# Performance work log

Measured on AMD Instinct MI355X. Metric: run time of the kernel, lower is better.

## Reference

```python
import jax, jax.numpy as jnp
import numpy as np

H = 16  # num_heads
D = 64  # head_dim


def setup_inputs() -> dict:
    key = jax.random.key(0)
    ks = jax.random.split(key, 9)
    B, S, E = 2, 2048, 1024
    scale = 1.0 / np.sqrt(E)
    return {
        "hidden_states": jax.random.normal(ks[0], (B, S, E), jnp.float32),
        "bias": jax.random.normal(ks[1], (1, H, S, S), jnp.float32) * 0.02,
        "Wq": jax.random.normal(ks[2], (E, E), jnp.float32) * scale,
        "bq": jax.random.normal(ks[3], (E,), jnp.float32) * 0.02,
        "Wk": jax.random.normal(ks[4], (E, E), jnp.float32) * scale,
        "bk": jax.random.normal(ks[5], (E,), jnp.float32) * 0.02,
        "Wv": jax.random.normal(ks[6], (E, E), jnp.float32) * scale,
        "bv": jax.random.normal(ks[7], (E,), jnp.float32) * 0.02,
        "Wo": jax.random.normal(ks[8], (E, E), jnp.float32) * scale,
    }


def _split_heads(x, B, S):
    # (B, S, E) -> (B, H, S, D)
    return x.reshape(B, S, H, D).transpose(0, 2, 1, 3)


def reference(hidden_states, bias, Wq, bq, Wk, bk, Wv, bv, Wo):
    B, S, E = hidden_states.shape
    # nn.Linear: y = x @ W^T + b
    q = _split_heads(hidden_states @ Wq.T + bq, B, S)
    k = _split_heads(hidden_states @ Wk.T + bk, B, S)
    v = _split_heads(hidden_states @ Wv.T + bv, B, S)
    scores = jnp.einsum("bhqd,bhkd->bhqk", q, k) / jnp.sqrt(jnp.asarray(D, q.dtype))
    scores = scores + bias  # bias [1,H,S,S] broadcasts over batch (matches .repeat)
    attn = jax.nn.softmax(scores, axis=-1)
    out = jnp.einsum("bhqk,bhkd->bhqd", attn, v)
    out = out.transpose(0, 2, 1, 3).reshape(B, S, E)
    return out @ Wo.T
```

## Files before the change

kernel.cpp:

```cpp
#include <hip/hip_runtime.h>
#include <hip/hip_bf16.h>


typedef __attribute__((ext_vector_type(8))) __bf16 bf16x8;
typedef __attribute__((ext_vector_type(4))) float f32x4;

__device__ __forceinline__ void gl2lds16(const void* g, void* l) {
    __builtin_amdgcn_global_load_lds(
        (const __attribute__((address_space(1))) void*)g,
        (__attribute__((address_space(3))) void*)l, 16, 0, 0);
}

__global__ __launch_bounds__(256) void prep(
    const float* __restrict__ hs, const float* __restrict__ Wq,
    const float* __restrict__ Wk, const float* __restrict__ Wv,
    const float* __restrict__ Wo,
    __bf16* __restrict__ hsb, __bf16* __restrict__ wqb, __bf16* __restrict__ wkb,
    __bf16* __restrict__ wvb, __bf16* __restrict__ wohb, __bf16* __restrict__ wolb)
{
    size_t i = (size_t)blockIdx.x * 256 + threadIdx.x;
    const float* s; __bf16 *d1, *d2 = nullptr; size_t off;
    if (i < 1048576)      { s = hs; d1 = hsb; off = i; }
    else if (i < 1310720) { s = Wq; d1 = wqb; off = i - 1048576; }
    else if (i < 1572864) { s = Wk; d1 = wkb; off = i - 1310720; }
    else if (i < 1835008) { s = Wv; d1 = wvb; off = i - 1572864; }
    else                  { s = Wo; d1 = wohb; d2 = wolb; off = i - 1835008; }
    float4 v = *(const float4*)(s + off * 4);
    union { __bf16 b[4]; uint2 u; } ph;
    ph.b[0] = (__bf16)v.x; ph.b[1] = (__bf16)v.y;
    ph.b[2] = (__bf16)v.z; ph.b[3] = (__bf16)v.w;
    *(uint2*)(d1 + off * 4) = ph.u;
    if (d2) {
        union { __bf16 b[4]; uint2 u; } pl;
        pl.b[0] = (__bf16)(v.x - (float)ph.b[0]);
        pl.b[1] = (__bf16)(v.y - (float)ph.b[1]);
        pl.b[2] = (__bf16)(v.z - (float)ph.b[2]);
        pl.b[3] = (__bf16)(v.w - (float)ph.b[3]);
        *(uint2*)(d2 + off * 4) = pl.u;
    }
}

__global__ __launch_bounds__(256, 3) void gemm_qkv(
    const __bf16* __restrict__ hsb, const __bf16* __restrict__ wqb,
    const __bf16* __restrict__ wkb, const __bf16* __restrict__ wvb,
    const float* __restrict__ bq, const float* __restrict__ bk, const float* __restrict__ bv,
    __bf16* __restrict__ qo, __bf16* __restrict__ ko, __bf16* __restrict__ vTo)
{
    __shared__ alignas(16) __bf16 As[128][32];
    __shared__ alignas(16) __bf16 Ws[128][32];
    const int tid = threadIdx.x;
    const int w = tid >> 6, lane = tid & 63, quad = lane >> 4, l = lane & 15;
    const int blk = blockIdx.x;
    const int proj = blk >> 8;
    const int loc = blk & 255;
    int bm, bn;
    const __bf16 *Ap, *Wp; const float* bp;
    if (proj == 0)      { Ap = hsb; Wp = wqb; bp = bq; bm = (loc >> 3) << 7; bn = (loc & 7) << 7; }
    else if (proj == 1) { Ap = hsb; Wp = wkb; bp = bk; bm = (loc >> 3) << 7; bn = (loc & 7) << 7; }
    else                { Ap = wvb; Wp = hsb; bp = bv; bm = (loc & 7) << 7; bn = (loc >> 3) << 7; }
    const int wm = (w >> 1) << 6, wn = (w & 1) << 6;
    const int seg_r = lane >> 2, seg_c = (lane & 3) << 3;

    f32x4 acc[4][4];
#pragma unroll
    for (int i = 0; i < 4; ++i)
#pragma unroll
        for (int j = 0; j < 4; ++j) acc[i][j] = f32x4{0.f, 0.f, 0.f, 0.f};

    for (int k0 = 0; k0 < 1024; k0 += 32) {
        __syncthreads();
#pragma unroll
        for (int j = 0; j < 2; ++j) {
            int seg = w * 2 + j;
            int row = seg * 16 + seg_r;
            gl2lds16(Ap + (size_t)(bm + row) * 1024 + k0 + seg_c,
                     (char*)As + seg * 1024 + lane * 16);
            gl2lds16(Wp + (size_t)(bn + row) * 1024 + k0 + seg_c,
                     (char*)Ws + seg * 1024 + lane * 16);
        }
        __syncthreads();
        bf16x8 af[4], bfr[4];
#pragma unroll
        for (int t = 0; t < 4; ++t) {
            af[t]  = *(const bf16x8*)&As[wm + t * 16 + l][quad * 8];
            bfr[t] = *(const bf16x8*)&Ws[wn + t * 16 + l][quad * 8];
        }
#pragma unroll
        for (int mt = 0; mt < 4; ++mt)
#pragma unroll
            for (int nt = 0; nt < 4; ++nt)
                acc[mt][nt] = __builtin_amdgcn_mfma_f32_16x16x32_bf16(
                    af[mt], bfr[nt], acc[mt][nt], 0, 0, 0);
    }

    if (proj < 2) {
        __bf16* dst = proj ? ko : qo;
        const float scale = proj ? 1.0f : 0.125f;
        float bcol[4];
#pragma unroll
        for (int nt = 0; nt < 4; ++nt) bcol[nt] = bp[bn + wn + nt * 16 + l];
#pragma unroll
        for (int mt = 0; mt < 4; ++mt)
#pragma unroll
            for (int r = 0; r < 4; ++r) {
                int m = bm + wm + mt * 16 + quad * 4 + r;
                int b_ = m >> 11, s = m & 2047;
#pragma unroll
                for (int nt = 0; nt < 4; ++nt) {
                    int n = bn + wn + nt * 16 + l;
                    int h = n >> 6, d = n & 63;
                    dst[(((size_t)(b_ * 16 + h) * 2048 + s) << 6) + d] =
                        (__bf16)((acc[mt][nt][r] + bcol[nt]) * scale);
                }
            }
    } else {
#pragma unroll
        for (int mt = 0; mt < 4; ++mt)
#pragma unroll
            for (int r = 0; r < 4; ++r) {
                int im = bm + wm + mt * 16 + quad * 4 + r;
                int h = im >> 6, d = im & 63;
                float bm_ = bp[im];
#pragma unroll
                for (int nt = 0; nt < 4; ++nt) {
                    int in = bn + wn + nt * 16 + l;
                    int b_ = in >> 11, s = in & 2047;
                    vTo[(((size_t)(b_ * 16 + h) * 64 + d) << 11) + s] =
                        (__bf16)(acc[mt][nt][r] + bm_);
                }
            }
    }
}

__global__ __launch_bounds__(256, 2) void flash_attn_mfma(
    const __bf16* __restrict__ q, const __bf16* __restrict__ k,
    const __bf16* __restrict__ vT, const float* __restrict__ bias,
    __bf16* __restrict__ attn_hi, __bf16* __restrict__ attn_lo)
{
    constexpr int S = 2048;
    __shared__ alignas(16) unsigned char smem[33792];
    __bf16 (*Ks)[64]  = (__bf16(*)[64])(smem);
    __bf16 (*VTs)[64] = (__bf16(*)[64])(smem + 8192);
    __bf16 (*Ps)[68]  = (__bf16(*)[68])(smem + 16384);
    __bf16 (*Qs)[64]  = (__bf16(*)[64])(smem + 16384);

    const int tid = threadIdx.x;
    const int b = blockIdx.x, h = blockIdx.y, qt = blockIdx.z;
    const int bh = b * 16 + h;
    const int q0 = qt * 128;
    const int w = tid >> 6, lane = tid & 63, quad = lane >> 4, l = lane & 15;

    const __bf16* Qp = q + ((size_t)bh * S + q0) * 64;
#pragma unroll
    for (int j = 0; j < 4; ++j) {
        int P = (w * 4 + j) * 64 + lane;
        int row = P >> 3, pblk = P & 7;
        int lblk = pblk ^ (row & 7);
        gl2lds16(Qp + row * 64 + lblk * 8, (char*)Qs + (size_t)P * 16);
    }
    __syncthreads();

    bf16x8 qf[2][2];
#pragma unroll
    for (int rt = 0; rt < 2; ++rt)
#pragma unroll
        for (int ks = 0; ks < 2; ++ks) {
            int row = w * 32 + rt * 16 + l;
            qf[rt][ks] = *(const bf16x8*)&Qs[row][((ks * 4 + quad) ^ (row & 7)) * 8];
        }

    float l_[2][4];
    f32x4 o_[2][4];
#pragma unroll
    for (int rt = 0; rt < 2; ++rt)
#pragma unroll
        for (int r = 0; r < 4; ++r) {
            l_[rt][r] = 0.0f;
            o_[rt][r] = f32x4{0.f, 0.f, 0.f, 0.f};
        }

    const __bf16* Kp0 = k + (size_t)bh * S * 64;
    const __bf16* Vp0 = vT + (size_t)bh * 64 * S;
    const float* Bp0 = bias + (size_t)h * S * S + (size_t)q0 * S;

    for (int kt = 0; kt < S / 64; ++kt) {
        f32x4 sc[2][4];
#pragma unroll
        for (int rt = 0; rt < 2; ++rt)
#pragma unroll
            for (int r = 0; r < 4; ++r) {
                const float* bp = Bp0 + (size_t)(w * 32 + rt * 16 + quad * 4 + r) * S
                                + kt * 64 + l;
#pragma unroll
                for (int ct = 0; ct < 4; ++ct) sc[rt][ct][r] = bp[ct * 16];
            }

        __syncthreads();
        const __bf16* Kt = Kp0 + kt * 64 * 64;
        const __bf16* Vt = Vp0 + kt * 64;
#pragma unroll
        for (int j = 0; j < 2; ++j) {
            int P = (w * 2 + j) * 64 + lane;
            int row = P >> 3, pblk = P & 7;
            int lblk = pblk ^ (row & 7);
            gl2lds16(Kt + row * 64 + lblk * 8,        (char*)Ks  + (size_t)P * 16);
            gl2lds16(Vt + (size_t)row * S + lblk * 8, (char*)VTs + (size_t)P * 16);
        }
        __syncthreads();

#pragma unroll
        for (int ct = 0; ct < 4; ++ct) {
            int krow = ct * 16 + l;
            bf16x8 b0 = *(const bf16x8*)&Ks[krow][((0 + quad) ^ (l & 7)) * 8];
            bf16x8 b1 = *(const bf16x8*)&Ks[krow][((4 + quad) ^ (l & 7)) * 8];
            sc[0][ct] = __builtin_amdgcn_mfma_f32_16x16x32_bf16(qf[0][0], b0, sc[0][ct], 0, 0, 0);
            sc[0][ct] = __builtin_amdgcn_mfma_f32_16x16x32_bf16(qf[0][1], b1, sc[0][ct], 0, 0, 0);
            sc[1][ct] = __builtin_amdgcn_mfma_f32_16x16x32_bf16(qf[1][0], b0, sc[1][ct], 0, 0, 0);
            sc[1][ct] = __builtin_amdgcn_mfma_f32_16x16x32_bf16(qf[1][1], b1, sc[1][ct], 0, 0, 0);
        }

#pragma unroll
        for (int rt = 0; rt < 2; ++rt)
#pragma unroll
            for (int r = 0; r < 4; ++r) {
                int row = w * 32 + rt * 16 + quad * 4 + r;
                float ps = 0.f;
#pragma unroll
                for (int ct = 0; ct < 4; ++ct) {
                    float p = __expf(sc[rt][ct][r] - 8.0f);
                    Ps[row][ct * 16 + l] = (__bf16)p;
                    ps += p;
                }
                l_[rt][r] += ps;
            }

#pragma unroll
        for (int ks = 0; ks < 2; ++ks) {
            bf16x8 pa0 = *(const bf16x8*)&Ps[w * 32 + l][ks * 32 + quad * 8];
            bf16x8 pa1 = *(const bf16x8*)&Ps[w * 32 + 16 + l][ks * 32 + quad * 8];
#pragma unroll
            for (int dt = 0; dt < 4; ++dt) {
                bf16x8 vb = *(const bf16x8*)&VTs[dt * 16 + l][((ks * 4 + quad) ^ (l & 7)) * 8];
                o_[0][dt] = __builtin_amdgcn_mfma_f32_16x16x32_bf16(pa0, vb, o_[0][dt], 0, 0, 0);
                o_[1][dt] = __builtin_amdgcn_mfma_f32_16x16x32_bf16(pa1, vb, o_[1][dt], 0, 0, 0);
            }
        }
    }

#pragma unroll
    for (int rt = 0; rt < 2; ++rt)
#pragma unroll
        for (int r = 0; r < 4; ++r) {
            float ps = l_[rt][r];
            ps += __shfl_xor(ps, 1);
            ps += __shfl_xor(ps, 2);
            ps += __shfl_xor(ps, 4);
            ps += __shfl_xor(ps, 8);
            float linv = 1.0f / ps;
            int row = q0 + w * 32 + rt * 16 + quad * 4 + r;
            size_t base = (size_t)(b * S + row) * 1024 + h * 64;
#pragma unroll
            for (int dt = 0; dt < 4; ++dt) {
                float x = o_[rt][dt][r] * linv;
                __bf16 hi = (__bf16)x;
                attn_hi[base + dt * 16 + l] = hi;
                attn_lo[base + dt * 16 + l] = (__bf16)(x - (float)hi);
            }
        }
}

__global__ __launch_bounds__(256, 3) void gemm_out(
    const __bf16* __restrict__ ah, const __bf16* __restrict__ al,
    const __bf16* __restrict__ wh, const __bf16* __restrict__ wl,
    float* __restrict__ C)
{
    __shared__ alignas(16) __bf16 Ah[64][32], Al[64][32];
    __shared__ alignas(16) __bf16 Wh[128][32], Wl[128][32];
    const int tid = threadIdx.x;
    const int w = tid >> 6, lane = tid & 63, quad = lane >> 4, l = lane & 15;
    const int bm = (int)(blockIdx.x >> 3) << 6;
    const int bn = (int)(blockIdx.x & 7) << 7;
    const int wm = (w >> 1) << 5, wn = (w & 1) << 6;
    const int seg_r = lane >> 2, seg_c = (lane & 3) << 3;

    f32x4 acc[2][4];
#pragma unroll
    for (int i = 0; i < 2; ++i)
#pragma unroll
        for (int j = 0; j < 4; ++j) acc[i][j] = f32x4{0.f, 0.f, 0.f, 0.f};

    for (int k0 = 0; k0 < 1024; k0 += 32) {
        __syncthreads();
        {
            int row = w * 16 + seg_r;
            gl2lds16(ah + (size_t)(bm + row) * 1024 + k0 + seg_c,
                     (char*)Ah + w * 1024 + lane * 16);
            gl2lds16(al + (size_t)(bm + row) * 1024 + k0 + seg_c,
                     (char*)Al + w * 1024 + lane * 16);
#pragma unroll
            for (int j = 0; j < 2; ++j) {
                int seg = w * 2 + j;
                int wrow = seg * 16 + seg_r;
                gl2lds16(wh + (size_t)(bn + wrow) * 1024 + k0 + seg_c,
                         (char*)Wh + seg * 1024 + lane * 16);
                gl2lds16(wl + (size_t)(bn + wrow) * 1024 + k0 + seg_c,
                         (char*)Wl + seg * 1024 + lane * 16);
            }
        }
        __syncthreads();
        bf16x8 ahf[2], alf[2], whf[4], wlf[4];
#pragma unroll
        for (int t = 0; t < 2; ++t) {
            ahf[t] = *(const bf16x8*)&Ah[wm + t * 16 + l][quad * 8];
            alf[t] = *(const bf16x8*)&Al[wm + t * 16 + l][quad * 8];
        }
#pragma unroll
        for (int t = 0; t < 4; ++t) {
            whf[t] = *(const bf16x8*)&Wh[wn + t * 16 + l][quad * 8];
            wlf[t] = *(const bf16x8*)&Wl[wn + t * 16 + l][quad * 8];
        }
#pragma unroll
        for (int mt = 0; mt < 2; ++mt)
#pragma unroll
            for (int nt = 0; nt < 4; ++nt) {
                acc[mt][nt] = __builtin_amdgcn_mfma_f32_16x16x32_bf16(ahf[mt], whf[nt], acc[mt][nt], 0, 0, 0);
                acc[mt][nt] = __builtin_amdgcn_mfma_f32_16x16x32_bf16(ahf[mt], wlf[nt], acc[mt][nt], 0, 0, 0);
                acc[mt][nt] = __builtin_amdgcn_mfma_f32_16x16x32_bf16(alf[mt], whf[nt], acc[mt][nt], 0, 0, 0);
            }
    }

#pragma unroll
    for (int mt = 0; mt < 2; ++mt)
#pragma unroll
        for (int r = 0; r < 4; ++r) {
            int m = bm + wm + mt * 16 + quad * 4 + r;
#pragma unroll
            for (int nt = 0; nt < 4; ++nt)
                C[(size_t)m * 1024 + bn + wn + nt * 16 + l] = acc[mt][nt][r];
        }
}

extern "C" void kernel_launch(void* const* d_in, const int* in_sizes, int n_in,
                              void* d_out, int out_size, void* d_ws, size_t ws_size,
                              hipStream_t stream) {
    const float* hs   = (const float*)d_in[0];
    const float* bias = (const float*)d_in[1];
    const float* Wq   = (const float*)d_in[2];
    const float* bq   = (const float*)d_in[3];
    const float* Wk   = (const float*)d_in[4];
    const float* bk   = (const float*)d_in[5];
    const float* Wv   = (const float*)d_in[6];
    const float* bv   = (const float*)d_in[7];
    const float* Wo   = (const float*)d_in[8];
    float* out = (float*)d_out;
    char* ws = (char*)d_ws;

    __bf16* attn_hi = (__bf16*)(ws);
    __bf16* attn_lo = (__bf16*)(ws + ((size_t) 8 << 20));
    __bf16* qb      = (__bf16*)(ws + ((size_t)16 << 20));
    __bf16* kb      = (__bf16*)(ws + ((size_t)24 << 20));
    __bf16* vTb     = (__bf16*)(ws + ((size_t)32 << 20));
    __bf16* hsb     = (__bf16*)(ws + ((size_t)40 << 20));
    __bf16* wqb     = (__bf16*)(ws + ((size_t)48 << 20));
    __bf16* wkb     = (__bf16*)(ws + ((size_t)50 << 20));
    __bf16* wvb     = (__bf16*)(ws + ((size_t)52 << 20));
    __bf16* wohb    = (__bf16*)(ws + ((size_t)54 << 20));
    __bf16* wolb    = (__bf16*)(ws + ((size_t)56 << 20));

    prep<<<8192, 256, 0, stream>>>(hs, Wq, Wk, Wv, Wo, hsb, wqb, wkb, wvb, wohb, wolb);

    gemm_qkv<<<768, 256, 0, stream>>>(hsb, wqb, wkb, wvb, bq, bk, bv, qb, kb, vTb);

    dim3 fg(2, 16, 16);
    flash_attn_mfma<<<fg, 256, 0, stream>>>(qb, kb, vTb, bias, attn_hi, attn_lo);

    gemm_out<<<512, 256, 0, stream>>>(attn_hi, attn_lo, wohb, wolb, out);
}
```

Measured before the change: 503.5 us.

## Double-buffer LDS staging across QKV GEMM, attention, and output GEMM

Converts the QKV projection and output GEMMs to a double-buffered LDS pipeline with K-step 64 and XOR-swizzled layout, so the next tile is prefetched while MFMAs run on the current one. The output GEMM tile shrinks to 64x64 and the grid doubles. In flash attention, K/V tiles are double-buffered in LDS and the bias slice for the next tile is prefetched into registers, which removes one barrier per iteration. In exchange, LDS use and register pressure go up, so occupancy hints are lowered.

```diff
diff --git a/kernel.cpp b/kernel.cpp
--- a/kernel.cpp
+++ b/kernel.cpp
@@ -40,14 +40,14 @@
     }
 }
 
-__global__ __launch_bounds__(256, 3) void gemm_qkv(
+__global__ __launch_bounds__(256, 2) void gemm_qkv(
     const __bf16* __restrict__ hsb, const __bf16* __restrict__ wqb,
     const __bf16* __restrict__ wkb, const __bf16* __restrict__ wvb,
     const float* __restrict__ bq, const float* __restrict__ bk, const float* __restrict__ bv,
     __bf16* __restrict__ qo, __bf16* __restrict__ ko, __bf16* __restrict__ vTo)
 {
-    __shared__ alignas(16) __bf16 As[128][32];
-    __shared__ alignas(16) __bf16 Ws[128][32];
+    __shared__ alignas(16) __bf16 As[2][128][64];
+    __shared__ alignas(16) __bf16 Ws[2][128][64];
     const int tid = threadIdx.x;
     const int w = tid >> 6, lane = tid & 63, quad = lane >> 4, l = lane & 15;
     const int blk = blockIdx.x;
@@ -59,7 +59,19 @@
     else if (proj == 1) { Ap = hsb; Wp = wkb; bp = bk; bm = (loc >> 3) << 7; bn = (loc & 7) << 7; }
     else                { Ap = wvb; Wp = hsb; bp = bv; bm = (loc & 7) << 7; bn = (loc >> 3) << 7; }
     const int wm = (w >> 1) << 6, wn = (w & 1) << 6;
-    const int seg_r = lane >> 2, seg_c = (lane & 3) << 3;
+
+    auto stage = [&](int it, int buf) {
+#pragma unroll
+        for (int j = 0; j < 4; ++j) {
+            int flat = j * 256 + tid;
+            int row = flat >> 3, p = flat & 7;
+            int col = ((p ^ (row & 7)) << 3);
+            gl2lds16(Ap + (size_t)(bm + row) * 1024 + it * 64 + col,
+                     (char*)As + buf * 16384 + flat * 16);
+            gl2lds16(Wp + (size_t)(bn + row) * 1024 + it * 64 + col,
+                     (char*)Ws + buf * 16384 + flat * 16);
+        }
+    };
 
     f32x4 acc[4][4];
 #pragma unroll
@@ -67,30 +79,29 @@
 #pragma unroll
         for (int j = 0; j < 4; ++j) acc[i][j] = f32x4{0.f, 0.f, 0.f, 0.f};
 
-    for (int k0 = 0; k0 < 1024; k0 += 32) {
+    stage(0, 0);
+    for (int it = 0; it < 16; ++it) {
+        const int cur = it & 1;
+        asm volatile("s_waitcnt vmcnt(0)" ::: "memory");
         __syncthreads();
-#pragma unroll
-        for (int j = 0; j < 2; ++j) {
-            int seg = w * 2 + j;
-            int row = seg * 16 + seg_r;
-            gl2lds16(Ap + (size_t)(bm + row) * 1024 + k0 + seg_c,
-                     (char*)As + seg * 1024 + lane * 16);
-            gl2lds16(Wp + (size_t)(bn + row) * 1024 + k0 + seg_c,
-                     (char*)Ws + seg * 1024 + lane * 16);
-        }
-        __syncthreads();
-        bf16x8 af[4], bfr[4];
-#pragma unroll
-        for (int t = 0; t < 4; ++t) {
-            af[t]  = *(const bf16x8*)&As[wm + t * 16 + l][quad * 8];
-            bfr[t] = *(const bf16x8*)&Ws[wn + t * 16 + l][quad * 8];
-        }
+        if (it < 15) stage(it + 1, cur ^ 1);
+        bf16x8 af[4][2], bfr[4][2];
+#pragma unroll
+        for (int t = 0; t < 4; ++t)
+#pragma unroll
+            for (int ks = 0; ks < 2; ++ks) {
+                int ra = wm + t * 16 + l;
+                int rb = wn + t * 16 + l;
+                af[t][ks]  = *(const bf16x8*)&As[cur][ra][(((ks * 4 + quad) ^ (ra & 7)) << 3)];
+                bfr[t][ks] = *(const bf16x8*)&Ws[cur][rb][(((ks * 4 + quad) ^ (rb & 7)) << 3)];
+            }
 #pragma unroll
         for (int mt = 0; mt < 4; ++mt)
 #pragma unroll
-            for (int nt = 0; nt < 4; ++nt)
-                acc[mt][nt] = __builtin_amdgcn_mfma_f32_16x16x32_bf16(
-                    af[mt], bfr[nt], acc[mt][nt], 0, 0, 0);
+            for (int nt = 0; nt < 4; ++nt) {
+                acc[mt][nt] = __builtin_amdgcn_mfma_f32_16x16x32_bf16(af[mt][0], bfr[nt][0], acc[mt][nt], 0, 0, 0);
+                acc[mt][nt] = __builtin_amdgcn_mfma_f32_16x16x32_bf16(af[mt][1], bfr[nt][1], acc[mt][nt], 0, 0, 0);
+            }
     }
 
     if (proj < 2) {
@@ -138,11 +149,8 @@
     __bf16* __restrict__ attn_hi, __bf16* __restrict__ attn_lo)
 {
     constexpr int S = 2048;
-    __shared__ alignas(16) unsigned char smem[33792];
-    __bf16 (*Ks)[64]  = (__bf16(*)[64])(smem);
-    __bf16 (*VTs)[64] = (__bf16(*)[64])(smem + 8192);
-    __bf16 (*Ps)[68]  = (__bf16(*)[68])(smem + 16384);
-    __bf16 (*Qs)[64]  = (__bf16(*)[64])(smem + 16384);
+    __shared__ alignas(16) unsigned char smem[50176];
+    __bf16 (*Ps)[68] = (__bf16(*)[68])(smem + 32768);
 
     const int tid = threadIdx.x;
     const int b = blockIdx.x, h = blockIdx.y, qt = blockIdx.z;
@@ -150,14 +158,46 @@
     const int q0 = qt * 128;
     const int w = tid >> 6, lane = tid & 63, quad = lane >> 4, l = lane & 15;
 
-    const __bf16* Qp = q + ((size_t)bh * S + q0) * 64;
+    const __bf16* Qp  = q + ((size_t)bh * S + q0) * 64;
+    const __bf16* Kp0 = k + (size_t)bh * S * 64;
+    const __bf16* Vp0 = vT + (size_t)bh * 64 * S;
+    const float*  Bp0 = bias + (size_t)h * S * S + (size_t)q0 * S;
+
+    auto stageKV = [&](int kt, int buf) {
+#pragma unroll
+        for (int j = 0; j < 2; ++j) {
+            int flat = j * 256 + tid;
+            int row = flat >> 3, p = flat & 7;
+            int col = ((p ^ (row & 7)) << 3);
+            gl2lds16(Kp0 + (size_t)kt * 4096 + row * 64 + col,
+                     (char*)smem + buf * 8192 + flat * 16);
+            gl2lds16(Vp0 + (size_t)kt * 64 + (size_t)row * S + col,
+                     (char*)smem + 16384 + buf * 8192 + flat * 16);
+        }
+    };
+    auto loadBias = [&](int kt, float* dst) {
+#pragma unroll
+        for (int rt = 0; rt < 2; ++rt)
+#pragma unroll
+            for (int r = 0; r < 4; ++r) {
+                const float* bp = Bp0 + (size_t)(w * 32 + rt * 16 + quad * 4 + r) * S
+                                + kt * 64 + l;
+#pragma unroll
+                for (int ct = 0; ct < 4; ++ct) dst[(rt * 4 + r) * 4 + ct] = bp[ct * 16];
+            }
+    };
+
+    float bc[32], bnx[32];
+    loadBias(0, bc);
+    stageKV(0, 0);
 #pragma unroll
     for (int j = 0; j < 4; ++j) {
-        int P = (w * 4 + j) * 64 + lane;
-        int row = P >> 3, pblk = P & 7;
-        int lblk = pblk ^ (row & 7);
-        gl2lds16(Qp + row * 64 + lblk * 8, (char*)Qs + (size_t)P * 16);
-    }
+        int flat = j * 256 + tid;
+        int row = flat >> 3, p = flat & 7;
+        int col = ((p ^ (row & 7)) << 3);
+        gl2lds16(Qp + row * 64 + col, (char*)smem + 32768 + flat * 16);
+    }
+    asm volatile("s_waitcnt vmcnt(0)" ::: "memory");
     __syncthreads();
 
     bf16x8 qf[2][2];
@@ -166,7 +206,8 @@
 #pragma unroll
         for (int ks = 0; ks < 2; ++ks) {
             int row = w * 32 + rt * 16 + l;
-            qf[rt][ks] = *(const bf16x8*)&Qs[row][((ks * 4 + quad) ^ (row & 7)) * 8];
+            qf[rt][ks] = *(const bf16x8*)((char*)smem + 32768 + row * 128
+                                          + (((ks * 4 + quad) ^ (row & 7)) << 4));
         }
 
     float l_[2][4];
@@ -179,40 +220,29 @@
             o_[rt][r] = f32x4{0.f, 0.f, 0.f, 0.f};
         }
 
-    const __bf16* Kp0 = k + (size_t)bh * S * 64;
-    const __bf16* Vp0 = vT + (size_t)bh * 64 * S;
-    const float* Bp0 = bias + (size_t)h * S * S + (size_t)q0 * S;
-
-    for (int kt = 0; kt < S / 64; ++kt) {
+#pragma unroll 2
+    for (int kt = 0; kt < 32; ++kt) {
+        const int cur = kt & 1;
+        if (kt < 31) {
+            loadBias(kt + 1, bnx);
+            stageKV(kt + 1, cur ^ 1);
+        }
+
         f32x4 sc[2][4];
 #pragma unroll
         for (int rt = 0; rt < 2; ++rt)
 #pragma unroll
-            for (int r = 0; r < 4; ++r) {
-                const float* bp = Bp0 + (size_t)(w * 32 + rt * 16 + quad * 4 + r) * S
-                                + kt * 64 + l;
-#pragma unroll
-                for (int ct = 0; ct < 4; ++ct) sc[rt][ct][r] = bp[ct * 16];
-            }
-
-        __syncthreads();
-        const __bf16* Kt = Kp0 + kt * 64 * 64;
-        const __bf16* Vt = Vp0 + kt * 64;
-#pragma unroll
-        for (int j = 0; j < 2; ++j) {
-            int P = (w * 2 + j) * 64 + lane;
-            int row = P >> 3, pblk = P & 7;
-            int lblk = pblk ^ (row & 7);
-            gl2lds16(Kt + row * 64 + lblk * 8,        (char*)Ks  + (size_t)P * 16);
-            gl2lds16(Vt + (size_t)row * S + lblk * 8, (char*)VTs + (size_t)P * 16);
-        }
-        __syncthreads();
+            for (int r = 0; r < 4; ++r)
+#pragma unroll
+                for (int ct = 0; ct < 4; ++ct) sc[rt][ct][r] = bc[(rt * 4 + r) * 4 + ct];
 
 #pragma unroll
         for (int ct = 0; ct < 4; ++ct) {
             int krow = ct * 16 + l;
-            bf16x8 b0 = *(const bf16x8*)&Ks[krow][((0 + quad) ^ (l & 7)) * 8];
-            bf16x8 b1 = *(const bf16x8*)&Ks[krow][((4 + quad) ^ (l & 7)) * 8];
+            bf16x8 b0 = *(const bf16x8*)((char*)smem + cur * 8192 + krow * 128
+                                         + (((0 + quad) ^ (krow & 7)) << 4));
+            bf16x8 b1 = *(const bf16x8*)((char*)smem + cur * 8192 + krow * 128
+                                         + (((4 + quad) ^ (krow & 7)) << 4));
             sc[0][ct] = __builtin_amdgcn_mfma_f32_16x16x32_bf16(qf[0][0], b0, sc[0][ct], 0, 0, 0);
             sc[0][ct] = __builtin_amdgcn_mfma_f32_16x16x32_bf16(qf[0][1], b1, sc[0][ct], 0, 0, 0);
             sc[1][ct] = __builtin_amdgcn_mfma_f32_16x16x32_bf16(qf[1][0], b0, sc[1][ct], 0, 0, 0);
@@ -240,11 +270,18 @@
             bf16x8 pa1 = *(const bf16x8*)&Ps[w * 32 + 16 + l][ks * 32 + quad * 8];
 #pragma unroll
             for (int dt = 0; dt < 4; ++dt) {
-                bf16x8 vb = *(const bf16x8*)&VTs[dt * 16 + l][((ks * 4 + quad) ^ (l & 7)) * 8];
+                int vrow = dt * 16 + l;
+                bf16x8 vb = *(const bf16x8*)((char*)smem + 16384 + cur * 8192 + vrow * 128
+                                             + (((ks * 4 + quad) ^ (vrow & 7)) << 4));
                 o_[0][dt] = __builtin_amdgcn_mfma_f32_16x16x32_bf16(pa0, vb, o_[0][dt], 0, 0, 0);
                 o_[1][dt] = __builtin_amdgcn_mfma_f32_16x16x32_bf16(pa1, vb, o_[1][dt], 0, 0, 0);
             }
         }
+
+#pragma unroll
+        for (int i = 0; i < 32; ++i) bc[i] = bnx[i];
+        asm volatile("s_waitcnt vmcnt(0)" ::: "memory");
+        __syncthreads();
     }
 
 #pragma unroll
@@ -269,64 +306,70 @@
         }
 }
 
-__global__ __launch_bounds__(256, 3) void gemm_out(
+__global__ __launch_bounds__(256, 2) void gemm_out(
     const __bf16* __restrict__ ah, const __bf16* __restrict__ al,
     const __bf16* __restrict__ wh, const __bf16* __restrict__ wl,
     float* __restrict__ C)
 {
-    __shared__ alignas(16) __bf16 Ah[64][32], Al[64][32];
-    __shared__ alignas(16) __bf16 Wh[128][32], Wl[128][32];
+    __shared__ alignas(16) __bf16 Ah[2][64][64], Al[2][64][64];
+    __shared__ alignas(16) __bf16 Wh[2][64][64], Wl[2][64][64];
     const int tid = threadIdx.x;
     const int w = tid >> 6, lane = tid & 63, quad = lane >> 4, l = lane & 15;
-    const int bm = (int)(blockIdx.x >> 3) << 6;
-    const int bn = (int)(blockIdx.x & 7) << 7;
-    const int wm = (w >> 1) << 5, wn = (w & 1) << 6;
-    const int seg_r = lane >> 2, seg_c = (lane & 3) << 3;
-
-    f32x4 acc[2][4];
+    const int bm = (int)(blockIdx.x >> 4) << 6;
+    const int bn = (int)(blockIdx.x & 15) << 6;
+    const int wm = (w >> 1) << 5, wn = (w & 1) << 5;
+
+    auto stage = [&](int it, int buf) {
+#pragma unroll
+        for (int j = 0; j < 2; ++j) {
+            int flat = j * 256 + tid;
+            int row = flat >> 3, p = flat & 7;
+            int col = ((p ^ (row & 7)) << 3);
+            size_t ao = (size_t)(bm + row) * 1024 + it * 64 + col;
+            size_t wo = (size_t)(bn + row) * 1024 + it * 64 + col;
+            gl2lds16(ah + ao, (char*)Ah + buf * 8192 + flat * 16);
+            gl2lds16(al + ao, (char*)Al + buf * 8192 + flat * 16);
+            gl2lds16(wh + wo, (char*)Wh + buf * 8192 + flat * 16);
+            gl2lds16(wl + wo, (char*)Wl + buf * 8192 + flat * 16);
+        }
+    };
+
+    f32x4 acc[2][2];
 #pragma unroll
     for (int i = 0; i < 2; ++i)
 #pragma unroll
-        for (int j = 0; j < 4; ++j) acc[i][j] = f32x4{0.f, 0.f, 0.f, 0.f};
-
-    for (int k0 = 0; k0 < 1024; k0 += 32) {
+        for (int j = 0; j < 2; ++j) acc[i][j] = f32x4{0.f, 0.f, 0.f, 0.f};
+
+    stage(0, 0);
+    for (int it = 0; it < 16; ++it) {
+        const int cur = it & 1;
+        asm volatile("s_waitcnt vmcnt(0)" ::: "memory");
         __syncthreads();
-        {
-            int row = w * 16 + seg_r;
-            gl2lds16(ah + (size_t)(bm + row) * 1024 + k0 + seg_c,
-                     (char*)Ah + w * 1024 + lane * 16);
-            gl2lds16(al + (size_t)(bm + row) * 1024 + k0 + seg_c,
-                     (char*)Al + w * 1024 + lane * 16);
-#pragma unroll
-            for (int j = 0; j < 2; ++j) {
-                int seg = w * 2 + j;
-                int wrow = seg * 16 + seg_r;
-                gl2lds16(wh + (size_t)(bn + wrow) * 1024 + k0 + seg_c,
-                         (char*)Wh + seg * 1024 + lane * 16);
-                gl2lds16(wl + (size_t)(bn + wrow) * 1024 + k0 + seg_c,
-                         (char*)Wl + seg * 1024 + lane * 16);
-            }
-        }
-        __syncthreads();
-        bf16x8 ahf[2], alf[2], whf[4], wlf[4];
-#pragma unroll
-        for (int t = 0; t < 2; ++t) {
-            ahf[t] = *(const bf16x8*)&Ah[wm + t * 16 + l][quad * 8];
-            alf[t] = *(const bf16x8*)&Al[wm + t * 16 + l][quad * 8];
-        }
-#pragma unroll
-        for (int t = 0; t < 4; ++t) {
-            whf[t] = *(const bf16x8*)&Wh[wn + t * 16 + l][quad * 8];
-            wlf[t] = *(const bf16x8*)&Wl[wn + t * 16 + l][quad * 8];
-        }
+        if (it < 15) stage(it + 1, cur ^ 1);
+        bf16x8 ahf[2][2], alf[2][2], whf[2][2], wlf[2][2];
+#pragma unroll
+        for (int t = 0; t < 2; ++t)
+#pragma unroll
+            for (int ks = 0; ks < 2; ++ks) {
+                int ra = wm + t * 16 + l;
+                int rb = wn + t * 16 + l;
+                int ca = (((ks * 4 + quad) ^ (ra & 7)) << 3);
+                int cb = (((ks * 4 + quad) ^ (rb & 7)) << 3);
+                ahf[t][ks] = *(const bf16x8*)&Ah[cur][ra][ca];
+                alf[t][ks] = *(const bf16x8*)&Al[cur][ra][ca];
+                whf[t][ks] = *(const bf16x8*)&Wh[cur][rb][cb];
+                wlf[t][ks] = *(const bf16x8*)&Wl[cur][rb][cb];
+            }
 #pragma unroll
         for (int mt = 0; mt < 2; ++mt)
 #pragma unroll
-            for (int nt = 0; nt < 4; ++nt) {
-                acc[mt][nt] = __builtin_amdgcn_mfma_f32_16x16x32_bf16(ahf[mt], whf[nt], acc[mt][nt], 0, 0, 0);
-                acc[mt][nt] = __builtin_amdgcn_mfma_f32_16x16x32_bf16(ahf[mt], wlf[nt], acc[mt][nt], 0, 0, 0);
-                acc[mt][nt] = __builtin_amdgcn_mfma_f32_16x16x32_bf16(alf[mt], whf[nt], acc[mt][nt], 0, 0, 0);
-            }
+            for (int nt = 0; nt < 2; ++nt)
+#pragma unroll
+                for (int ks = 0; ks < 2; ++ks) {
+                    acc[mt][nt] = __builtin_amdgcn_mfma_f32_16x16x32_bf16(ahf[mt][ks], whf[nt][ks], acc[mt][nt], 0, 0, 0);
+                    acc[mt][nt] = __builtin_amdgcn_mfma_f32_16x16x32_bf16(ahf[mt][ks], wlf[nt][ks], acc[mt][nt], 0, 0, 0);
+                    acc[mt][nt] = __builtin_amdgcn_mfma_f32_16x16x32_bf16(alf[mt][ks], whf[nt][ks], acc[mt][nt], 0, 0, 0);
+                }
     }
 
 #pragma unroll
@@ -335,7 +378,7 @@
         for (int r = 0; r < 4; ++r) {
             int m = bm + wm + mt * 16 + quad * 4 + r;
 #pragma unroll
-            for (int nt = 0; nt < 4; ++nt)
+            for (int nt = 0; nt < 2; ++nt)
                 C[(size_t)m * 1024 + bn + wn + nt * 16 + l] = acc[mt][nt][r];
         }
 }
@@ -374,5 +417,5 @@
     dim3 fg(2, 16, 16);
     flash_attn_mfma<<<fg, 256, 0, stream>>>(qb, kb, vTb, bias, attn_hi, attn_lo);
 
-    gemm_out<<<512, 256, 0, stream>>>(attn_hi, attn_lo, wohb, wolb, out);
-}
+    gemm_out<<<1024, 256, 0, stream>>>(attn_hi, attn_lo, wohb, wolb, out);
+}
```

Result: slower. 533.0 us (+5.8%).
